# Kernel optimization log

Hardware: AMD Instinct MI355X
Metric: run time of the kernel (lower is better)

Reference implementation:

```python
import jax, jax.numpy as jnp
import numpy as np

N_NODES = 100000
N_EDGES = 1600000
BN_EPS = 1e-5
NUM_LAYER = 20


def setup_inputs() -> dict:
    key = jax.random.key(0)
    ks = jax.random.split(key, 10)
    inp = {
        "M": jax.random.normal(ks[0], (N_NODES, 3), dtype=jnp.float32),
        "H": jax.random.normal(ks[1], (N_EDGES, 3), dtype=jnp.float32),
        "edge_index": jax.random.randint(ks[2], (2, N_EDGES), 0, N_NODES, dtype=jnp.int32),
        # mlp_e: Linear(9,4) -> BN(4) -> ReLU -> Linear(4,3)
        "we_w1": jax.random.normal(ks[3], (9, 4), dtype=jnp.float32) * 0.3,
        "we_b1": jnp.zeros((4,), jnp.float32),
        "we_g1": jnp.ones((4,), jnp.float32),
        "we_be1": jnp.zeros((4,), jnp.float32),
        "we_w2": jax.random.normal(ks[4], (4, 3), dtype=jnp.float32) * 0.3,
        "we_b2": jnp.zeros((3,), jnp.float32),
        # mlp_v: Linear(6,3) -> BN(3) -> ReLU -> Linear(3,3)
        "wv_w1": jax.random.normal(ks[5], (6, 3), dtype=jnp.float32) * 0.3,
        "wv_b1": jnp.zeros((3,), jnp.float32),
        "wv_g1": jnp.ones((3,), jnp.float32),
        "wv_be1": jnp.zeros((3,), jnp.float32),
        "wv_w2": jax.random.normal(ks[6], (3, 3), dtype=jnp.float32) * 0.3,
        "wv_b2": jnp.zeros((3,), jnp.float32),
        # head: Linear(3,3) -> BN(3) -> ReLU -> Linear(3,2) -> Softmax
        "out_w1": jax.random.normal(ks[7], (3, 3), dtype=jnp.float32) * 0.3,
        "out_b1": jnp.zeros((3,), jnp.float32),
        "out_g": jnp.ones((3,), jnp.float32),
        "out_be": jnp.zeros((3,), jnp.float32),
        "out_w2": jax.random.normal(ks[8], (3, 2), dtype=jnp.float32) * 0.3,
        "out_b2": jnp.zeros((2,), jnp.float32),
    }
    return inp


def _bn(x, g, b):
    # BatchNorm1d in training mode: batch stats, biased variance
    m = jnp.mean(x, axis=0)
    v = jnp.mean(jnp.square(x - m), axis=0)
    return (x - m) * jax.lax.rsqrt(v + BN_EPS) * g + b


def reference(M, H, edge_index, we_w1, we_b1, we_g1, we_be1, we_w2, we_b2,
              wv_w1, wv_b1, wv_g1, wv_be1, wv_w2, wv_b2,
              out_w1, out_b1, out_g, out_be, out_w2, out_b2):
    src = edge_index[0]  # _j (source, flow=source_to_target)
    dst = edge_index[1]  # _i (target), also the aggregation index
    n = M.shape[0]

    def layer(carry, _):
        M, H = carry
        Mi = M[dst]  # [E,3] gather of target node feats
        Mj = M[src]  # [E,3] gather of source node feats
        e_in = jnp.concatenate([Mi, Mj, H], axis=1)  # [E,9]
        Hn = jax.nn.relu(_bn(e_in @ we_w1 + we_b1, we_g1, we_be1)) @ we_w2 + we_b2  # [E,3]
        v_in = jnp.concatenate([Mi, Hn], axis=1)  # [E,6]
        Mmsg = jax.nn.relu(_bn(v_in @ wv_w1 + wv_b1, wv_g1, wv_be1)) @ wv_w2 + wv_b2  # [E,3]
        Mn = jax.ops.segment_sum(Mmsg, dst, num_segments=n)  # scatter-add to targets
        return (Mn, Hn), None

    (M, H), _ = jax.lax.scan(layer, (M, H), None, length=NUM_LAYER)
    logits = jax.nn.relu(_bn(H @ out_w1 + out_b1, out_g, out_be)) @ out_w2 + out_b2  # [E,2]
    return jax.nn.softmax(logits, axis=1)
```

## Files before the change

kernel.cpp:

```cpp
#include <hip/hip_runtime.h>
#include <hip/hip_fp16.h>
#include <math.h>

#define NNODES 100000
#define NEDGES 1600000
#define NGROUP (NEDGES / 4)
#define NLAYERS 20
#define NB 256
#define BLK 256
#define GRIDE 1024
#define STRIDE (GRIDE * BLK)
#define GRIDL ((NGROUP + BLK - 1) / BLK)
#define NBLKN ((NNODES + 255) / 256)
#define GRIDN4 ((NNODES * 4 + BLK - 1) / BLK)

struct __align__(8) H4 { __half h[4]; };

template<int N>
__device__ __forceinline__ void block_stats_atomic(const float* vals, double* base) {
  __shared__ float sm[8][4];
  int lane = threadIdx.x & 63, wid = threadIdx.x >> 6;
  __syncthreads();
  #pragma unroll
  for (int n = 0; n < N; ++n) {
    float d = vals[n];
    #pragma unroll
    for (int o = 32; o > 0; o >>= 1) d += __shfl_down(d, o, 64);
    if (lane == 0) sm[n][wid] = d;
  }
  __syncthreads();
  if (threadIdx.x < N) {
    double s = (double)sm[threadIdx.x][0] + (double)sm[threadIdx.x][1]
             + (double)sm[threadIdx.x][2] + (double)sm[threadIdx.x][3];
    atomicAdd(base + threadIdx.x, s);
  }
}

template<int NS>
__device__ __forceinline__ void bank_reduce(const double* __restrict__ acc, double* res) {
  __shared__ double part[4][8];
  int t = threadIdx.x;
  double v[NS];
  #pragma unroll
  for (int s = 0; s < NS; ++s) v[s] = acc[t * 8 + s];
  #pragma unroll
  for (int o = 32; o > 0; o >>= 1)
    #pragma unroll
    for (int s = 0; s < NS; ++s) v[s] += __shfl_down(v[s], o, 64);
  if ((t & 63) == 0) {
    int w = t >> 6;
    #pragma unroll
    for (int s = 0; s < NS; ++s) part[w][s] = v[s];
  }
  __syncthreads();
  #pragma unroll
  for (int s = 0; s < NS; ++s) res[s] = part[0][s] + part[1][s] + part[2][s] + part[3][s];
}

__device__ __forceinline__ void compute_x(const float4 mi, const float4 mj,
    float h0, float h1, float h2,
    const float* __restrict__ w, const float* __restrict__ b, float* x) {
  #pragma unroll
  for (int j = 0; j < 4; ++j) {
    float t = b[j];
    t += mi.x * w[0 * 4 + j]; t += mi.y * w[1 * 4 + j]; t += mi.z * w[2 * 4 + j];
    t += mj.x * w[3 * 4 + j]; t += mj.y * w[4 * 4 + j]; t += mj.z * w[5 * 4 + j];
    t += h0 * w[6 * 4 + j];  t += h1 * w[7 * 4 + j];  t += h2 * w[8 * 4 + j];
    x[j] = t;
  }
}

__global__ void __launch_bounds__(BLK) kz(const float* __restrict__ Min,
                                          float* __restrict__ M,
                                          int* __restrict__ hist,
                                          double* __restrict__ accs) {
  int tid = blockIdx.x * BLK + threadIdx.x;
  for (int v = tid; v < NNODES; v += STRIDE) {
    float4 m;
    m.x = Min[3 * v]; m.y = Min[3 * v + 1]; m.z = Min[3 * v + 2]; m.w = 0.f;
    *(float4*)(M + 4 * (size_t)v) = m;
    hist[v] = 0;
  }
  for (int i = tid; i < 3 * NB * 8; i += STRIDE) accs[i] = 0.0;
}

__global__ void __launch_bounds__(BLK) khr(const int* __restrict__ dst,
                                           int* __restrict__ hist,
                                           int* __restrict__ rankpos) {
  int g = blockIdx.x * BLK + threadIdx.x;
  if (g >= NGROUP) return;
  int4 d4 = ((const int4*)dst)[g];
  int4 r;
  r.x = atomicAdd(&hist[d4.x], 1);
  r.y = atomicAdd(&hist[d4.y], 1);
  r.z = atomicAdd(&hist[d4.z], 1);
  r.w = atomicAdd(&hist[d4.w], 1);
  ((int4*)rankpos)[g] = r;
}

__global__ void __launch_bounds__(256) ksA(const int* __restrict__ hist,
                                           int* __restrict__ bsum) {
  __shared__ int sm[256];
  int i = blockIdx.x * 256 + threadIdx.x;
  sm[threadIdx.x] = (i < NNODES) ? hist[i] : 0;
  __syncthreads();
  for (int o = 128; o > 0; o >>= 1) {
    if (threadIdx.x < o) sm[threadIdx.x] += sm[threadIdx.x + o];
    __syncthreads();
  }
  if (threadIdx.x == 0) bsum[blockIdx.x] = sm[0];
}

__global__ void __launch_bounds__(512) ksB(const int* __restrict__ bsum,
                                           int* __restrict__ bbase) {
  __shared__ int sm[512];
  int t = threadIdx.x;
  sm[t] = (t < NBLKN) ? bsum[t] : 0;
  __syncthreads();
  for (int o = 1; o < 512; o <<= 1) {
    int v = (t >= o) ? sm[t - o] : 0;
    __syncthreads();
    sm[t] += v;
    __syncthreads();
  }
  if (t < NBLKN) bbase[t] = (t == 0) ? 0 : sm[t - 1];
}

__global__ void __launch_bounds__(256) ksC(const int* __restrict__ hist,
                                           const int* __restrict__ bbase,
                                           int* __restrict__ off,
                                           int* __restrict__ dp) {
  __shared__ int sm[256];
  int t = threadIdx.x;
  int i = blockIdx.x * 256 + t;
  int v = (i < NNODES) ? hist[i] : 0;
  sm[t] = v;
  __syncthreads();
  for (int o = 1; o < 256; o <<= 1) {
    int u = (t >= o) ? sm[t - o] : 0;
    __syncthreads();
    sm[t] += u;
    __syncthreads();
  }
  if (i < NNODES) {
    int ex = bbase[blockIdx.x] + sm[t] - v;
    off[i] = ex;
    for (int e = ex; e < ex + v; ++e) dp[e] = i;
  }
  if (i == 0) off[NNODES] = NEDGES;
}

__global__ void __launch_bounds__(BLK) kpk(const int* __restrict__ dp,
                                           int2* __restrict__ dpp) {
  int g = blockIdx.x * BLK + threadIdx.x;
  if (g >= NGROUP) return;
  int4 d4 = ((const int4*)dp)[g];
  int2 o;
  o.x = d4.x;
  o.y = (d4.y - d4.x) | ((d4.z - d4.x) << 8) | ((d4.w - d4.x) << 16);
  dpp[g] = o;
}

__global__ void __launch_bounds__(BLK) kp1(const int* __restrict__ dst,
                                           const int* __restrict__ off,
                                           int* __restrict__ rankpos,
                                           int* __restrict__ eperm) {
  int g = blockIdx.x * BLK + threadIdx.x;
  if (g >= NGROUP) return;
  int4 d4 = ((const int4*)dst)[g];
  int4 r4 = ((int4*)rankpos)[g];
  int4 p4;
  p4.x = off[d4.x] + r4.x;
  p4.y = off[d4.y] + r4.y;
  p4.z = off[d4.z] + r4.z;
  p4.w = off[d4.w] + r4.w;
  int e = 4 * g;
  eperm[p4.x] = e; eperm[p4.y] = e + 1; eperm[p4.z] = e + 2; eperm[p4.w] = e + 3;
  ((int4*)rankpos)[g] = p4;
}

__global__ void __launch_bounds__(BLK) kp2(const int* __restrict__ src,
                                           const float* __restrict__ Hin,
                                           const int* __restrict__ eperm,
                                           int* __restrict__ sp,
                                           __half* __restrict__ Hp) {
  int g = blockIdx.x * BLK + threadIdx.x;
  if (g >= NGROUP) return;
  int4 e4 = ((const int4*)eperm)[g];
  int4 s4;
  s4.x = src[e4.x];
  s4.y = src[e4.y];
  s4.z = src[e4.z];
  s4.w = src[e4.w];
  __half hh[12];
  int ee[4] = {e4.x, e4.y, e4.z, e4.w};
  #pragma unroll
  for (int k = 0; k < 4; ++k) {
    size_t e3 = 3 * (size_t)ee[k];
    hh[3 * k]     = __float2half(Hin[e3]);
    hh[3 * k + 1] = __float2half(Hin[e3 + 1]);
    hh[3 * k + 2] = __float2half(Hin[e3 + 2]);
  }
  ((int4*)sp)[g] = s4;
  H4* Hv = (H4*)(Hp + 12 * (size_t)g);
  H4 a, b, c;
  #pragma unroll
  for (int i = 0; i < 4; ++i) { a.h[i] = hh[i]; b.h[i] = hh[4 + i]; c.h[i] = hh[8 + i]; }
  Hv[0] = a; Hv[1] = b; Hv[2] = c;
}

__global__ void __launch_bounds__(BLK) k1(
    const float* __restrict__ M, const __half* __restrict__ H,
    __half* __restrict__ xb,
    const int* __restrict__ sp, const int2* __restrict__ dpp,
    const float* __restrict__ W1, const float* __restrict__ b1,
    double* __restrict__ acc1, double* __restrict__ acc2) {
  int g = blockIdx.x * BLK + threadIdx.x;
  if (blockIdx.x == 0)
    for (int i = threadIdx.x; i < NB * 8; i += BLK) acc2[i] = 0.0;

  float sx[4] = {0, 0, 0, 0}, sq[4] = {0, 0, 0, 0};
  if (g < NGROUP) {
    int4 s4 = ((const int4*)sp)[g];
    int2 dppg = dpp[g];
    int d0 = dppg.x;
    int d1 = d0 + (dppg.y & 255);
    int d2 = d0 + ((dppg.y >> 8) & 255);
    int d3 = d0 + ((dppg.y >> 16) & 255);
    const H4* Hv = (const H4*)(H + 12 * (size_t)g);
    H4 a = Hv[0], b = Hv[1], c = Hv[2];
    float hf[12];
    #pragma unroll
    for (int i = 0; i < 4; ++i) {
      hf[i] = __half2float(a.h[i]); hf[4 + i] = __half2float(b.h[i]); hf[8 + i] = __half2float(c.h[i]);
    }
    float4 mi0 = *(const float4*)(M + 4 * (size_t)d0);
    float4 mj0 = *(const float4*)(M + 4 * (size_t)s4.x);
    float4 mi1 = *(const float4*)(M + 4 * (size_t)d1);
    float4 mj1 = *(const float4*)(M + 4 * (size_t)s4.y);
    float4 mi2 = *(const float4*)(M + 4 * (size_t)d2);
    float4 mj2 = *(const float4*)(M + 4 * (size_t)s4.z);
    float4 mi3 = *(const float4*)(M + 4 * (size_t)d3);
    float4 mj3 = *(const float4*)(M + 4 * (size_t)s4.w);
    float x[4][4];
    compute_x(mi0, mj0, hf[0], hf[1], hf[2],  W1, b1, x[0]);
    compute_x(mi1, mj1, hf[3], hf[4], hf[5],  W1, b1, x[1]);
    compute_x(mi2, mj2, hf[6], hf[7], hf[8],  W1, b1, x[2]);
    compute_x(mi3, mj3, hf[9], hf[10], hf[11], W1, b1, x[3]);
    H4* xv = (H4*)xb + 4 * (size_t)g;
    #pragma unroll
    for (int k = 0; k < 4; ++k) {
      H4 xo;
      #pragma unroll
      for (int j = 0; j < 4; ++j) {
        __half hx = __float2half(x[k][j]);
        xo.h[j] = hx;
        float xr = __half2float(hx);
        sx[j] += xr; sq[j] += xr * xr;
      }
      xv[k] = xo;
    }
  }
  float vals[8] = {sx[0], sx[1], sx[2], sx[3], sq[0], sq[1], sq[2], sq[3]};
  block_stats_atomic<8>(vals, acc1 + (size_t)(blockIdx.x & (NB - 1)) * 8);
}

__global__ void __launch_bounds__(BLK) k2(
    const float* __restrict__ M, __half* __restrict__ Hn,
    const __half* __restrict__ xb, const int2* __restrict__ dpp,
    const float* __restrict__ g1, const float* __restrict__ be1,
    const float* __restrict__ W2, const float* __restrict__ b2,
    const float* __restrict__ V1, const float* __restrict__ vb1,
    const double* __restrict__ acc1, double* __restrict__ acc2,
    int isFinal,
    const float* __restrict__ OW1, const float* __restrict__ ob1,
    double* __restrict__ accF) {
  double red[8];
  bank_reduce<8>(acc1, red);
  float s1[4], t1[4];
  {
    const double invE = 1.0 / (double)NEDGES;
    #pragma unroll
    for (int j = 0; j < 4; ++j) {
      double m = red[j] * invE;
      double var = red[4 + j] * invE - m * m;
      double sc = (double)g1[j] / sqrt(var + 1e-5);
      s1[j] = (float)sc;
      t1[j] = (float)((double)be1[j] - m * sc);
    }
  }
  float sz[3] = {0, 0, 0}, szz[3] = {0, 0, 0}, sf[3] = {0, 0, 0}, sff[3] = {0, 0, 0};
  int g = blockIdx.x * BLK + threadIdx.x;
  if (g < NGROUP) {
    int2 dppg = dpp[g];
    int dd[4];
    dd[0] = dppg.x;
    dd[1] = dd[0] + (dppg.y & 255);
    dd[2] = dd[0] + ((dppg.y >> 8) & 255);
    dd[3] = dd[0] + ((dppg.y >> 16) & 255);
    float4 mi[4];
    mi[0] = *(const float4*)(M + 4 * (size_t)dd[0]);
    mi[1] = *(const float4*)(M + 4 * (size_t)dd[1]);
    mi[2] = *(const float4*)(M + 4 * (size_t)dd[2]);
    mi[3] = *(const float4*)(M + 4 * (size_t)dd[3]);
    const H4* xv = (const H4*)xb + 4 * (size_t)g;
    __half hh[12];
    #pragma unroll
    for (int k = 0; k < 4; ++k) {
      H4 xh = xv[k];
      float y[4];
      #pragma unroll
      for (int j = 0; j < 4; ++j)
        y[j] = fmaxf(__half2float(xh.h[j]) * s1[j] + t1[j], 0.f);
      float hr[3];
      #pragma unroll
      for (int c = 0; c < 3; ++c) {
        float v = b2[c] + y[0] * W2[0 * 3 + c] + y[1] * W2[1 * 3 + c]
                        + y[2] * W2[2 * 3 + c] + y[3] * W2[3 * 3 + c];
        __half hv = __float2half(v);
        hh[3 * k + c] = hv;
        hr[c] = __half2float(hv);
      }
      #pragma unroll
      for (int c = 0; c < 3; ++c) {
        float z = vb1[c] + mi[k].x * V1[0 * 3 + c] + mi[k].y * V1[1 * 3 + c] + mi[k].z * V1[2 * 3 + c]
                         + hr[0] * V1[3 * 3 + c] + hr[1] * V1[4 * 3 + c] + hr[2] * V1[5 * 3 + c];
        sz[c] += z; szz[c] += z * z;
      }
      if (isFinal) {
        #pragma unroll
        for (int c = 0; c < 3; ++c) {
          float f = ob1[c] + hr[0] * OW1[0 * 3 + c] + hr[1] * OW1[1 * 3 + c] + hr[2] * OW1[2 * 3 + c];
          sf[c] += f; sff[c] += f * f;
        }
      }
    }
    H4* Hw = (H4*)(Hn + 12 * (size_t)g);
    H4 oA, oB, oC;
    #pragma unroll
    for (int i = 0; i < 4; ++i) { oA.h[i] = hh[i]; oB.h[i] = hh[4 + i]; oC.h[i] = hh[8 + i]; }
    Hw[0] = oA; Hw[1] = oB; Hw[2] = oC;
  }
  size_t bank = (size_t)(blockIdx.x & (NB - 1)) * 8;
  float v6[6] = {sz[0], sz[1], sz[2], szz[0], szz[1], szz[2]};
  block_stats_atomic<6>(v6, acc2 + bank);
  if (isFinal) {
    float v6b[6] = {sf[0], sf[1], sf[2], sff[0], sff[1], sff[2]};
    block_stats_atomic<6>(v6b, accF + bank);
  }
}

__global__ void __launch_bounds__(BLK) k3(
    float* __restrict__ M, const __half* __restrict__ Hn,
    const int* __restrict__ off,
    const float* __restrict__ V1, const float* __restrict__ vb1,
    const float* __restrict__ vg1, const float* __restrict__ vbe1,
    const float* __restrict__ V2, const float* __restrict__ vb2,
    const double* __restrict__ acc2, double* __restrict__ acc1) {
  double red[6];
  bank_reduce<6>(acc2, red);
  float s2[3], t2[3];
  {
    const double invE = 1.0 / (double)NEDGES;
    #pragma unroll
    for (int c = 0; c < 3; ++c) {
      double m = red[c] * invE;
      double var = red[3 + c] * invE - m * m;
      double sc = (double)vg1[c] / sqrt(var + 1e-5);
      s2[c] = (float)sc;
      t2[c] = (float)((double)vbe1[c] - m * sc);
    }
  }
  if (blockIdx.x == 0)
    for (int i = threadIdx.x; i < NB * 8; i += BLK) acc1[i] = 0.0;

  int idx = blockIdx.x * BLK + threadIdx.x;
  int v = idx >> 2, q = idx & 3;
  if (v >= NNODES) return;
  float4 mi = *(const float4*)(M + 4 * (size_t)v);
  int e0 = off[v], e1 = off[v + 1];
  float a0 = 0.f, a1 = 0.f, a2v = 0.f;
  for (int e = e0 + q; e < e1; e += 4) {
    size_t e3 = 3 * (size_t)e;
    float h0 = __half2float(Hn[e3]), h1 = __half2float(Hn[e3 + 1]), h2 = __half2float(Hn[e3 + 2]);
    float y[3];
    #pragma unroll
    for (int c = 0; c < 3; ++c) {
      float z = vb1[c] + mi.x * V1[0 * 3 + c] + mi.y * V1[1 * 3 + c] + mi.z * V1[2 * 3 + c]
                       + h0 * V1[3 * 3 + c] + h1 * V1[4 * 3 + c] + h2 * V1[5 * 3 + c];
      y[c] = fmaxf(z * s2[c] + t2[c], 0.f);
    }
    a0  += vb2[0] + y[0] * V2[0] + y[1] * V2[3] + y[2] * V2[6];
    a1  += vb2[1] + y[0] * V2[1] + y[1] * V2[4] + y[2] * V2[7];
    a2v += vb2[2] + y[0] * V2[2] + y[1] * V2[5] + y[2] * V2[8];
  }
  a0  += __shfl_down(a0, 2, 4);  a0  += __shfl_down(a0, 1, 4);
  a1  += __shfl_down(a1, 2, 4);  a1  += __shfl_down(a1, 1, 4);
  a2v += __shfl_down(a2v, 2, 4); a2v += __shfl_down(a2v, 1, 4);
  if (q == 0) {
    float4 o; o.x = a0; o.y = a1; o.z = a2v; o.w = 0.f;
    *(float4*)(M + 4 * (size_t)v) = o;
  }
}

__global__ void __launch_bounds__(BLK) f2(
    const __half* __restrict__ H, const int* __restrict__ pos,
    const float* __restrict__ OW1, const float* __restrict__ ob1,
    const float* __restrict__ og, const float* __restrict__ obe,
    const float* __restrict__ OW2, const float* __restrict__ ob2,
    const double* __restrict__ accF, float* __restrict__ out) {
  double red[6];
  bank_reduce<6>(accF, red);
  float sF[3], tF[3];
  {
    const double invE = 1.0 / (double)NEDGES;
    #pragma unroll
    for (int c = 0; c < 3; ++c) {
      double m = red[c] * invE;
      double var = red[3 + c] * invE - m * m;
      double sc = (double)og[c] / sqrt(var + 1e-5);
      sF[c] = (float)sc;
      tF[c] = (float)((double)obe[c] - m * sc);
    }
  }
  int g = blockIdx.x * BLK + threadIdx.x;
  if (g >= NGROUP) return;
  int4 p4 = ((const int4*)pos)[g];
  int p[4] = {p4.x, p4.y, p4.z, p4.w};
  float2 o[4];
  #pragma unroll
  for (int k = 0; k < 4; ++k) {
    size_t p3 = 3 * (size_t)p[k];
    float h0 = __half2float(H[p3]), h1 = __half2float(H[p3 + 1]), h2 = __half2float(H[p3 + 2]);
    float y[3];
    #pragma unroll
    for (int c = 0; c < 3; ++c) {
      float f = ob1[c] + h0 * OW1[0 * 3 + c] + h1 * OW1[1 * 3 + c] + h2 * OW1[2 * 3 + c];
      y[c] = fmaxf(f * sF[c] + tF[c], 0.f);
    }
    float l0 = ob2[0] + y[0] * OW2[0] + y[1] * OW2[2] + y[2] * OW2[4];
    float l1 = ob2[1] + y[0] * OW2[1] + y[1] * OW2[3] + y[2] * OW2[5];
    float mx = fmaxf(l0, l1);
    float e0 = __expf(l0 - mx), e1 = __expf(l1 - mx);
    float inv = 1.f / (e0 + e1);
    o[k].x = e0 * inv; o[k].y = e1 * inv;
  }
  float4 oA, oB;
  oA.x = o[0].x; oA.y = o[0].y; oA.z = o[1].x; oA.w = o[1].y;
  oB.x = o[2].x; oB.y = o[2].y; oB.z = o[3].x; oB.w = o[3].y;
  ((float4*)out)[2 * (size_t)g] = oA;
  ((float4*)out)[2 * (size_t)g + 1] = oB;
}

extern "C" void kernel_launch(void* const* d_in, const int* in_sizes, int n_in,
                              void* d_out, int out_size, void* d_ws, size_t ws_size,
                              hipStream_t stream) {
  const float* M_in   = (const float*)d_in[0];
  const float* H_in   = (const float*)d_in[1];
  const int*   ei     = (const int*)d_in[2];
  const float* we_w1  = (const float*)d_in[3];
  const float* we_b1  = (const float*)d_in[4];
  const float* we_g1  = (const float*)d_in[5];
  const float* we_be1 = (const float*)d_in[6];
  const float* we_w2  = (const float*)d_in[7];
  const float* we_b2  = (const float*)d_in[8];
  const float* wv_w1  = (const float*)d_in[9];
  const float* wv_b1  = (const float*)d_in[10];
  const float* wv_g1  = (const float*)d_in[11];
  const float* wv_be1 = (const float*)d_in[12];
  const float* wv_w2  = (const float*)d_in[13];
  const float* wv_b2  = (const float*)d_in[14];
  const float* out_w1 = (const float*)d_in[15];
  const float* out_b1 = (const float*)d_in[16];
  const float* out_g  = (const float*)d_in[17];
  const float* out_be = (const float*)d_in[18];
  const float* out_w2 = (const float*)d_in[19];
  const float* out_b2 = (const float*)d_in[20];
  const int* src = ei;
  const int* dst = ei + NEDGES;

  float* ws = (float*)d_ws;
  float* M    = ws;
  __half* Hp  = (__half*)(ws + 400000);
  __half* xb  = (__half*)(ws + 2800000);
  int* ib      = (int*)(ws + 6000000);
  int* sp      = ib;
  int* dp      = ib + 1600000;
  int* rankpos = ib + 3200000;
  int2* dpp    = (int2*)(ib + 4800000);
  int* hist    = ib + 5600000;
  int* off     = ib + 5700000;
  int* bsum    = ib + 5800001;
  int* bbase   = ib + 5800401;
  double* accs = (double*)(ws + 6000000 + 5800802);
  double* acc1 = accs;
  double* acc2 = accs + NB * 8;
  double* accF = accs + 2 * NB * 8;
  int* eperm   = dp;

  kz<<<GRIDE, BLK, 0, stream>>>(M_in, M, hist, accs);
  khr<<<GRIDL, BLK, 0, stream>>>(dst, hist, rankpos);
  ksA<<<NBLKN, 256, 0, stream>>>(hist, bsum);
  ksB<<<1, 512, 0, stream>>>(bsum, bbase);
  ksC<<<NBLKN, 256, 0, stream>>>(hist, bbase, off, dp);
  kpk<<<GRIDL, BLK, 0, stream>>>(dp, dpp);
  kp1<<<GRIDL, BLK, 0, stream>>>(dst, off, rankpos, eperm);
  kp2<<<GRIDL, BLK, 0, stream>>>(src, H_in, eperm, sp, Hp);

  for (int l = 0; l < NLAYERS; ++l) {
    k1<<<GRIDL, BLK, 0, stream>>>(M, Hp, xb, sp, dpp, we_w1, we_b1, acc1, acc2);
    k2<<<GRIDL, BLK, 0, stream>>>(M, Hp, xb, dpp, we_g1, we_be1,
                                  we_w2, we_b2, wv_w1, wv_b1, acc1, acc2,
                                  (l == NLAYERS - 1) ? 1 : 0, out_w1, out_b1, accF);
    if (l < NLAYERS - 1)
      k3<<<GRIDN4, BLK, 0, stream>>>(
          M, Hp, off, wv_w1, wv_b1, wv_g1, wv_be1, wv_w2, wv_b2, acc2, acc1);
  }
  f2<<<GRIDL, BLK, 0, stream>>>(Hp, rankpos, out_w1, out_b1, out_g, out_be,
                                out_w2, out_b2, accF, (float*)d_out);
}
```

Measured before the change: 1.151 ms.

## Pad edge H to four halves, process two groups per thread in k1

Stores each edge's H features padded to four halves (8-byte aligned) so k1, k3 and f2 can fetch one edge with a single 8-byte load instead of three scalar half loads. k1 now handles two 4-edge groups per thread, halving its grid. k3 hoists the node-dependent part of the first linear layer out of the edge loop and adds the bias once per edge count. H storage grows by a third and the workspace offsets move to make room.

Measured after the change: 1.239 ms. 1.08x slower.

```diff
diff --git a/kernel.cpp b/kernel.cpp
--- a/kernel.cpp
+++ b/kernel.cpp
@@ -11,6 +11,7 @@
 #define GRIDE 1024
 #define STRIDE (GRIDE * BLK)
 #define GRIDL ((NGROUP + BLK - 1) / BLK)
+#define GRIDL2 ((NGROUP / 2 + BLK - 1) / BLK)
 #define NBLKN ((NNODES + 255) / 256)
 #define GRIDN4 ((NNODES * 4 + BLK - 1) / BLK)
 
@@ -67,6 +68,18 @@
     t += mj.x * w[3 * 4 + j]; t += mj.y * w[4 * 4 + j]; t += mj.z * w[5 * 4 + j];
     t += h0 * w[6 * 4 + j];  t += h1 * w[7 * 4 + j];  t += h2 * w[8 * 4 + j];
     x[j] = t;
+  }
+}
+
+__device__ __forceinline__ void bn_coeff(const double* red, int n,
+    const float* g, const float* be, float* s, float* t) {
+  const double invE = 1.0 / (double)NEDGES;
+  for (int c = 0; c < n; ++c) {
+    double m = red[c] * invE;
+    double var = red[n + c] * invE - m * m;
+    double sc = (double)g[c] / sqrt(var + 1e-5);
+    s[c] = (float)sc;
+    t[c] = (float)((double)be[c] - m * sc);
   }
 }
 
@@ -192,21 +205,19 @@
   s4.y = src[e4.y];
   s4.z = src[e4.z];
   s4.w = src[e4.w];
-  __half hh[12];
+  ((int4*)sp)[g] = s4;
   int ee[4] = {e4.x, e4.y, e4.z, e4.w};
+  H4* Hv = (H4*)Hp + 4 * (size_t)g;
   #pragma unroll
   for (int k = 0; k < 4; ++k) {
     size_t e3 = 3 * (size_t)ee[k];
-    hh[3 * k]     = __float2half(Hin[e3]);
-    hh[3 * k + 1] = __float2half(Hin[e3 + 1]);
-    hh[3 * k + 2] = __float2half(Hin[e3 + 2]);
-  }
-  ((int4*)sp)[g] = s4;
-  H4* Hv = (H4*)(Hp + 12 * (size_t)g);
-  H4 a, b, c;
-  #pragma unroll
-  for (int i = 0; i < 4; ++i) { a.h[i] = hh[i]; b.h[i] = hh[4 + i]; c.h[i] = hh[8 + i]; }
-  Hv[0] = a; Hv[1] = b; Hv[2] = c;
+    H4 o;
+    o.h[0] = __float2half(Hin[e3]);
+    o.h[1] = __float2half(Hin[e3 + 1]);
+    o.h[2] = __float2half(Hin[e3 + 2]);
+    o.h[3] = __half(0.0f);
+    Hv[k] = o;
+  }
 }
 
 __global__ void __launch_bounds__(BLK) k1(
@@ -215,50 +226,50 @@
     const int* __restrict__ sp, const int2* __restrict__ dpp,
     const float* __restrict__ W1, const float* __restrict__ b1,
     double* __restrict__ acc1, double* __restrict__ acc2) {
-  int g = blockIdx.x * BLK + threadIdx.x;
+  int t = blockIdx.x * BLK + threadIdx.x;
   if (blockIdx.x == 0)
     for (int i = threadIdx.x; i < NB * 8; i += BLK) acc2[i] = 0.0;
 
   float sx[4] = {0, 0, 0, 0}, sq[4] = {0, 0, 0, 0};
-  if (g < NGROUP) {
-    int4 s4 = ((const int4*)sp)[g];
-    int2 dppg = dpp[g];
-    int d0 = dppg.x;
-    int d1 = d0 + (dppg.y & 255);
-    int d2 = d0 + ((dppg.y >> 8) & 255);
-    int d3 = d0 + ((dppg.y >> 16) & 255);
-    const H4* Hv = (const H4*)(H + 12 * (size_t)g);
-    H4 a = Hv[0], b = Hv[1], c = Hv[2];
-    float hf[12];
-    #pragma unroll
-    for (int i = 0; i < 4; ++i) {
-      hf[i] = __half2float(a.h[i]); hf[4 + i] = __half2float(b.h[i]); hf[8 + i] = __half2float(c.h[i]);
-    }
-    float4 mi0 = *(const float4*)(M + 4 * (size_t)d0);
-    float4 mj0 = *(const float4*)(M + 4 * (size_t)s4.x);
-    float4 mi1 = *(const float4*)(M + 4 * (size_t)d1);
-    float4 mj1 = *(const float4*)(M + 4 * (size_t)s4.y);
-    float4 mi2 = *(const float4*)(M + 4 * (size_t)d2);
-    float4 mj2 = *(const float4*)(M + 4 * (size_t)s4.z);
-    float4 mi3 = *(const float4*)(M + 4 * (size_t)d3);
-    float4 mj3 = *(const float4*)(M + 4 * (size_t)s4.w);
-    float x[4][4];
-    compute_x(mi0, mj0, hf[0], hf[1], hf[2],  W1, b1, x[0]);
-    compute_x(mi1, mj1, hf[3], hf[4], hf[5],  W1, b1, x[1]);
-    compute_x(mi2, mj2, hf[6], hf[7], hf[8],  W1, b1, x[2]);
-    compute_x(mi3, mj3, hf[9], hf[10], hf[11], W1, b1, x[3]);
-    H4* xv = (H4*)xb + 4 * (size_t)g;
-    #pragma unroll
-    for (int k = 0; k < 4; ++k) {
-      H4 xo;
+  int g0 = 2 * t;
+  if (g0 < NGROUP) {
+    #pragma unroll
+    for (int u = 0; u < 2; ++u) {
+      int g = g0 + u;
+      int4 s4 = ((const int4*)sp)[g];
+      int2 dg = dpp[g];
+      int d0 = dg.x;
+      int d1 = d0 + (dg.y & 255);
+      int d2 = d0 + ((dg.y >> 8) & 255);
+      int d3 = d0 + ((dg.y >> 16) & 255);
+      const H4* Hv = (const H4*)H + 4 * (size_t)g;
+      H4 h0 = Hv[0], h1 = Hv[1], h2 = Hv[2], h3 = Hv[3];
+      float4 mi0 = *(const float4*)(M + 4 * (size_t)d0);
+      float4 mj0 = *(const float4*)(M + 4 * (size_t)s4.x);
+      float4 mi1 = *(const float4*)(M + 4 * (size_t)d1);
+      float4 mj1 = *(const float4*)(M + 4 * (size_t)s4.y);
+      float4 mi2 = *(const float4*)(M + 4 * (size_t)d2);
+      float4 mj2 = *(const float4*)(M + 4 * (size_t)s4.z);
+      float4 mi3 = *(const float4*)(M + 4 * (size_t)d3);
+      float4 mj3 = *(const float4*)(M + 4 * (size_t)s4.w);
+      float x[4][4];
+      compute_x(mi0, mj0, __half2float(h0.h[0]), __half2float(h0.h[1]), __half2float(h0.h[2]), W1, b1, x[0]);
+      compute_x(mi1, mj1, __half2float(h1.h[0]), __half2float(h1.h[1]), __half2float(h1.h[2]), W1, b1, x[1]);
+      compute_x(mi2, mj2, __half2float(h2.h[0]), __half2float(h2.h[1]), __half2float(h2.h[2]), W1, b1, x[2]);
+      compute_x(mi3, mj3, __half2float(h3.h[0]), __half2float(h3.h[1]), __half2float(h3.h[2]), W1, b1, x[3]);
+      H4* xv = (H4*)xb + 4 * (size_t)g;
       #pragma unroll
-      for (int j = 0; j < 4; ++j) {
-        __half hx = __float2half(x[k][j]);
-        xo.h[j] = hx;
-        float xr = __half2float(hx);
-        sx[j] += xr; sq[j] += xr * xr;
+      for (int k = 0; k < 4; ++k) {
+        H4 xo;
+        #pragma unroll
+        for (int j = 0; j < 4; ++j) {
+          __half hx = __float2half(x[k][j]);
+          xo.h[j] = hx;
+          float xr = __half2float(hx);
+          sx[j] += xr; sq[j] += xr * xr;
+        }
+        xv[k] = xo;
       }
-      xv[k] = xo;
     }
   }
   float vals[8] = {sx[0], sx[1], sx[2], sx[3], sq[0], sq[1], sq[2], sq[3]};
@@ -278,33 +289,23 @@
   double red[8];
   bank_reduce<8>(acc1, red);
   float s1[4], t1[4];
-  {
-    const double invE = 1.0 / (double)NEDGES;
-    #pragma unroll
-    for (int j = 0; j < 4; ++j) {
-      double m = red[j] * invE;
-      double var = red[4 + j] * invE - m * m;
-      double sc = (double)g1[j] / sqrt(var + 1e-5);
-      s1[j] = (float)sc;
-      t1[j] = (float)((double)be1[j] - m * sc);
-    }
-  }
+  bn_coeff(red, 4, g1, be1, s1, t1);
   float sz[3] = {0, 0, 0}, szz[3] = {0, 0, 0}, sf[3] = {0, 0, 0}, sff[3] = {0, 0, 0};
   int g = blockIdx.x * BLK + threadIdx.x;
   if (g < NGROUP) {
-    int2 dppg = dpp[g];
+    int2 dg = dpp[g];
     int dd[4];
-    dd[0] = dppg.x;
-    dd[1] = dd[0] + (dppg.y & 255);
-    dd[2] = dd[0] + ((dppg.y >> 8) & 255);
-    dd[3] = dd[0] + ((dppg.y >> 16) & 255);
+    dd[0] = dg.x;
+    dd[1] = dd[0] + (dg.y & 255);
+    dd[2] = dd[0] + ((dg.y >> 8) & 255);
+    dd[3] = dd[0] + ((dg.y >> 16) & 255);
     float4 mi[4];
     mi[0] = *(const float4*)(M + 4 * (size_t)dd[0]);
     mi[1] = *(const float4*)(M + 4 * (size_t)dd[1]);
     mi[2] = *(const float4*)(M + 4 * (size_t)dd[2]);
     mi[3] = *(const float4*)(M + 4 * (size_t)dd[3]);
     const H4* xv = (const H4*)xb + 4 * (size_t)g;
-    __half hh[12];
+    H4* Hw = (H4*)Hn + 4 * (size_t)g;
     #pragma unroll
     for (int k = 0; k < 4; ++k) {
       H4 xh = xv[k];
@@ -312,15 +313,18 @@
       #pragma unroll
       for (int j = 0; j < 4; ++j)
         y[j] = fmaxf(__half2float(xh.h[j]) * s1[j] + t1[j], 0.f);
+      H4 ho;
       float hr[3];
       #pragma unroll
       for (int c = 0; c < 3; ++c) {
         float v = b2[c] + y[0] * W2[0 * 3 + c] + y[1] * W2[1 * 3 + c]
                         + y[2] * W2[2 * 3 + c] + y[3] * W2[3 * 3 + c];
         __half hv = __float2half(v);
-        hh[3 * k + c] = hv;
+        ho.h[c] = hv;
         hr[c] = __half2float(hv);
       }
+      ho.h[3] = __half(0.0f);
+      Hw[k] = ho;
       #pragma unroll
       for (int c = 0; c < 3; ++c) {
         float z = vb1[c] + mi[k].x * V1[0 * 3 + c] + mi[k].y * V1[1 * 3 + c] + mi[k].z * V1[2 * 3 + c]
@@ -335,11 +339,6 @@
         }
       }
     }
-    H4* Hw = (H4*)(Hn + 12 * (size_t)g);
-    H4 oA, oB, oC;
-    #pragma unroll
-    for (int i = 0; i < 4; ++i) { oA.h[i] = hh[i]; oB.h[i] = hh[4 + i]; oC.h[i] = hh[8 + i]; }
-    Hw[0] = oA; Hw[1] = oB; Hw[2] = oC;
   }
   size_t bank = (size_t)(blockIdx.x & (NB - 1)) * 8;
   float v6[6] = {sz[0], sz[1], sz[2], szz[0], szz[1], szz[2]};
@@ -360,17 +359,7 @@
   double red[6];
   bank_reduce<6>(acc2, red);
   float s2[3], t2[3];
-  {
-    const double invE = 1.0 / (double)NEDGES;
-    #pragma unroll
-    for (int c = 0; c < 3; ++c) {
-      double m = red[c] * invE;
-      double var = red[3 + c] * invE - m * m;
-      double sc = (double)vg1[c] / sqrt(var + 1e-5);
-      s2[c] = (float)sc;
-      t2[c] = (float)((double)vbe1[c] - m * sc);
-    }
-  }
+  bn_coeff(red, 3, vg1, vbe1, s2, t2);
   if (blockIdx.x == 0)
     for (int i = threadIdx.x; i < NB * 8; i += BLK) acc1[i] = 0.0;
 
@@ -378,22 +367,31 @@
   int v = idx >> 2, q = idx & 3;
   if (v >= NNODES) return;
   float4 mi = *(const float4*)(M + 4 * (size_t)v);
+  float zc[3];
+  #pragma unroll
+  for (int c = 0; c < 3; ++c)
+    zc[c] = vb1[c] + mi.x * V1[0 * 3 + c] + mi.y * V1[1 * 3 + c] + mi.z * V1[2 * 3 + c];
   int e0 = off[v], e1 = off[v + 1];
   float a0 = 0.f, a1 = 0.f, a2v = 0.f;
+  int cnt = 0;
+  const H4* Hq = (const H4*)Hn;
   for (int e = e0 + q; e < e1; e += 4) {
-    size_t e3 = 3 * (size_t)e;
-    float h0 = __half2float(Hn[e3]), h1 = __half2float(Hn[e3 + 1]), h2 = __half2float(Hn[e3 + 2]);
+    H4 hh = Hq[e];
+    float h0 = __half2float(hh.h[0]), h1 = __half2float(hh.h[1]), h2 = __half2float(hh.h[2]);
     float y[3];
     #pragma unroll
     for (int c = 0; c < 3; ++c) {
-      float z = vb1[c] + mi.x * V1[0 * 3 + c] + mi.y * V1[1 * 3 + c] + mi.z * V1[2 * 3 + c]
-                       + h0 * V1[3 * 3 + c] + h1 * V1[4 * 3 + c] + h2 * V1[5 * 3 + c];
+      float z = zc[c] + h0 * V1[3 * 3 + c] + h1 * V1[4 * 3 + c] + h2 * V1[5 * 3 + c];
       y[c] = fmaxf(z * s2[c] + t2[c], 0.f);
     }
-    a0  += vb2[0] + y[0] * V2[0] + y[1] * V2[3] + y[2] * V2[6];
-    a1  += vb2[1] + y[0] * V2[1] + y[1] * V2[4] + y[2] * V2[7];
-    a2v += vb2[2] + y[0] * V2[2] + y[1] * V2[5] + y[2] * V2[8];
-  }
+    a0  += y[0] * V2[0] + y[1] * V2[3] + y[2] * V2[6];
+    a1  += y[0] * V2[1] + y[1] * V2[4] + y[2] * V2[7];
+    a2v += y[0] * V2[2] + y[1] * V2[5] + y[2] * V2[8];
+    ++cnt;
+  }
+  a0  += vb2[0] * (float)cnt;
+  a1  += vb2[1] * (float)cnt;
+  a2v += vb2[2] * (float)cnt;
   a0  += __shfl_down(a0, 2, 4);  a0  += __shfl_down(a0, 1, 4);
   a1  += __shfl_down(a1, 2, 4);  a1  += __shfl_down(a1, 1, 4);
   a2v += __shfl_down(a2v, 2, 4); a2v += __shfl_down(a2v, 1, 4);
@@ -412,26 +410,17 @@
   double red[6];
   bank_reduce<6>(accF, red);
   float sF[3], tF[3];
-  {
-    const double invE = 1.0 / (double)NEDGES;
-    #pragma unroll
-    for (int c = 0; c < 3; ++c) {
-      double m = red[c] * invE;
-      double var = red[3 + c] * invE - m * m;
-      double sc = (double)og[c] / sqrt(var + 1e-5);
-      sF[c] = (float)sc;
-      tF[c] = (float)((double)obe[c] - m * sc);
-    }
-  }
+  bn_coeff(red, 3, og, obe, sF, tF);
   int g = blockIdx.x * BLK + threadIdx.x;
   if (g >= NGROUP) return;
   int4 p4 = ((const int4*)pos)[g];
   int p[4] = {p4.x, p4.y, p4.z, p4.w};
+  const H4* Hq = (const H4*)H;
   float2 o[4];
   #pragma unroll
   for (int k = 0; k < 4; ++k) {
-    size_t p3 = 3 * (size_t)p[k];
-    float h0 = __half2float(H[p3]), h1 = __half2float(H[p3 + 1]), h2 = __half2float(H[p3 + 2]);
+    H4 hh = Hq[p[k]];
+    float h0 = __half2float(hh.h[0]), h1 = __half2float(hh.h[1]), h2 = __half2float(hh.h[2]);
     float y[3];
     #pragma unroll
     for (int c = 0; c < 3; ++c) {
@@ -480,10 +469,10 @@
   const int* dst = ei + NEDGES;
 
   float* ws = (float*)d_ws;
-  float* M    = ws;
-  __half* Hp  = (__half*)(ws + 400000);
-  __half* xb  = (__half*)(ws + 2800000);
-  int* ib      = (int*)(ws + 6000000);
+  float* M     = ws;
+  __half* Hp   = (__half*)(ws + 400000);
+  __half* xb   = (__half*)(ws + 3600000);
+  int* ib      = (int*)(ws + 6800000);
   int* sp      = ib;
   int* dp      = ib + 1600000;
   int* rankpos = ib + 3200000;
@@ -492,7 +481,7 @@
   int* off     = ib + 5700000;
   int* bsum    = ib + 5800001;
   int* bbase   = ib + 5800401;
-  double* accs = (double*)(ws + 6000000 + 5800802);
+  double* accs = (double*)(ws + 6800000 + 5800802);
   double* acc1 = accs;
   double* acc2 = accs + NB * 8;
   double* accF = accs + 2 * NB * 8;
@@ -508,7 +497,7 @@
   kp2<<<GRIDL, BLK, 0, stream>>>(src, H_in, eperm, sp, Hp);
 
   for (int l = 0; l < NLAYERS; ++l) {
-    k1<<<GRIDL, BLK, 0, stream>>>(M, Hp, xb, sp, dpp, we_w1, we_b1, acc1, acc2);
+    k1<<<GRIDL2, BLK, 0, stream>>>(M, Hp, xb, sp, dpp, we_w1, we_b1, acc1, acc2);
     k2<<<GRIDL, BLK, 0, stream>>>(M, Hp, xb, dpp, we_g1, we_be1,
                                   we_w2, we_b2, wv_w1, wv_b1, acc1, acc2,
                                   (l == NLAYERS - 1) ? 1 : 0, out_w1, out_b1, accF);
```
